# Kernel optimization log

Hardware: AMD Instinct MI355X
Metric: run time of the kernel (lower is better)

## Reference

```python
import jax, jax.numpy as jnp
import numpy as np

G, N, D, K, OUT = 2048, 64, 128, 128, 10  # K*D == input_dim == 16384

def setup_inputs() -> dict:
    key = jax.random.key(0)
    k1, k2, k3, k4, k5 = jax.random.split(key, 5)
    x = jax.random.normal(k1, (G, N, D), dtype=jnp.float32)
    # nn.Linear(node_dim, input_dim/node_dim): weight [K, D], bias [K]
    W_att = jax.random.normal(k2, (K, D), dtype=jnp.float32) * (1.0 / np.sqrt(D))
    b_att = jax.random.normal(k3, (K,), dtype=jnp.float32) * 0.01
    # nn.Linear(input_dim, output_dim): weight [OUT, K*D], bias [OUT]
    W1 = jax.random.normal(k4, (OUT, K * D), dtype=jnp.float32) * (1.0 / np.sqrt(K * D))
    b1 = jax.random.normal(k5, (OUT,), dtype=jnp.float32) * 0.01
    return {"x": x, "W_att": W_att, "b_att": b_att, "W1": W1, "b1": b1}

def reference(x, W_att, b_att, W1, b1):
    # Per-graph gram matrix X^T X : [G, D, D], quantized to 2 decimals
    gram = jnp.einsum('gnd,gne->gde', x, x)
    gram = jnp.round(gram * 100.0) / 100.0
    # attend: Linear(D -> K) applied row-wise to gram -> attn_coef [G, D, K]
    attn = jnp.einsum('gde,ke->gdk', gram, W_att) + b_att
    # attn_weights = attn^T ([G, K, D]); pooled = attn_weights @ gram -> [G, K, D]
    pooled = jnp.einsum('gdk,gde->gke', attn, gram)
    flat = pooled.reshape(x.shape[0], K * D)  # view(input_dim)
    # linear1 (dropout omitted: eval mode)
    return flat @ W1.T + b1
```

## Files before the change

### kernel.cpp

```cpp
#include <hip/hip_runtime.h>

typedef __attribute__((ext_vector_type(8)))  __bf16    bf16x8;
typedef __attribute__((ext_vector_type(4)))  __bf16    bf16x4;
typedef __attribute__((ext_vector_type(16))) float     f32x16;
typedef __attribute__((ext_vector_type(4)))  _Float16  f16x4;
typedef __attribute__((ext_vector_type(2)))  __fp16    h16x2;
typedef __attribute__((ext_vector_type(8)))  __fp16    h16x8;

constexpr int NG  = 2048;
constexpr int NN  = 64;
constexpr int DD  = 128;
constexpr int KK  = 128;
constexpr int OUTD = 10;

__device__ __host__ inline void tileOf(int t, int& ti, int& tj) {
    if (t < 4)      { ti = 0; tj = t;     }
    else if (t < 7) { ti = 1; tj = t - 3; }
    else if (t < 9) { ti = 2; tj = t - 5; }
    else            { ti = 3; tj = 3;     }
}

__device__ inline int xtIdx(int r, int c) { return r * 64  + (c ^ ((r & 7) << 3)); }
__device__ inline int gIdx (int r, int c) { return r * 128 + (c ^ ((r & 15) << 3)); }

#if __has_builtin(__builtin_amdgcn_fdot2)
__device__ __forceinline__ float dot2f(h16x2 a, h16x2 b, float c) {
    return __builtin_amdgcn_fdot2(a, b, c, false);
}
#else
__device__ __forceinline__ float dot2f(h16x2 a, h16x2 b, float c) {
    return c + (float)a[0] * (float)b[0] + (float)a[1] * (float)b[1];
}
#endif

__global__ __launch_bounds__(256)
void fused_sp_kernel(const float* __restrict__ Wa,
                     const float* __restrict__ b_att,
                     const float* __restrict__ W1,
                     _Float16* __restrict__ Sp,
                     float* __restrict__ cgout)
{
    const int blk = blockIdx.x;
    const int o = blk / 10, t = blk - o * 10;
    int ti, tj; tileOf(t, ti, tj);
    const int Fi = ti * 32, Ej = tj * 32;
    const float* __restrict__ W1o = W1 + (size_t)o * (KK * DD);

    __shared__ float WaF[KK][32];
    __shared__ float WaE[KK][32];
    __shared__ float W1F[KK][32];
    __shared__ float W1E[KK][32];
    __shared__ float AFE[32][33];
    __shared__ float AEF[32][33];
    __shared__ float bsh[KK];

    const int tid = threadIdx.x;

    for (int r0 = 0; r0 < KK; r0 += 8) {
        const int r = r0 + (tid >> 5), cc = tid & 31;
        WaF[r][cc] = Wa[r * DD + Fi + cc];
        WaE[r][cc] = Wa[r * DD + Ej + cc];
        W1F[r][cc] = W1o[r * DD + Fi + cc];
        W1E[r][cc] = W1o[r * DD + Ej + cc];
    }
    if (tid < KK) bsh[tid] = b_att[tid];
    __syncthreads();

    {
        const int rloc = tid >> 3;
        const int q    = (tid & 7) * 4;
        float a0 = 0.f, a1 = 0.f, a2 = 0.f, a3 = 0.f;
        float b0 = 0.f, b1 = 0.f, b2 = 0.f, b3 = 0.f;
        for (int k = 0; k < KK; ++k) {
            const float av = WaF[k][rloc];
            const float4 wv = *(const float4*)&W1E[k][q];
            a0 += av * wv.x; a1 += av * wv.y; a2 += av * wv.z; a3 += av * wv.w;
            const float bv = WaE[k][rloc];
            const float4 vv = *(const float4*)&W1F[k][q];
            b0 += bv * vv.x; b1 += bv * vv.y; b2 += bv * vv.z; b3 += bv * vv.w;
        }
        AFE[rloc][q] = a0; AFE[rloc][q + 1] = a1; AFE[rloc][q + 2] = a2; AFE[rloc][q + 3] = a3;
        AEF[rloc][q] = b0; AEF[rloc][q + 1] = b1; AEF[rloc][q + 2] = b2; AEF[rloc][q + 3] = b3;
    }
    __syncthreads();

    {
        const int l  = tid & 63;
        const int rq = tid >> 6;
        const int eg = l & 31;
        const int e  = Ej + eg;
        f16x4 p;
#pragma unroll
        for (int j = 0; j < 4; ++j) {
            const int fl = j + 8 * rq + 4 * (l >> 5);
            const int f  = Fi + fl;
            float v;
            if (f < e)       v = AFE[fl][eg] + AEF[eg][fl];
            else if (f == e) v = AFE[fl][eg];
            else             v = 0.f;
            p[j] = (_Float16)v;
        }
        *(f16x4*)&Sp[(size_t)((o * 10 + t) * 64 + l) * 16 + rq * 4] = p;
    }

    if (ti == 0 && tid < 32) {
        float s = 0.f;
        for (int k = 0; k < KK; ++k) s += bsh[k] * W1E[k][tid];
        cgout[o * DD + Ej + tid] = s;
    }
}

__device__ __forceinline__ void process_graph(
    const float* __restrict__ xg,
    __bf16* __restrict__ XtL, __bf16* __restrict__ GL,
    float (*__restrict__ sp)[DD], float* __restrict__ sOut,
    int tid, int w, int l, int l31, int l5, int extraBase,
    f32x16& hacc0, f32x16& haccX)
{
    {
        const int f = tid & 127, half = tid >> 7;
#pragma unroll
        for (int ch = 0; ch < 2; ++ch) {
            float v[8];
#pragma unroll
            for (int i = 0; i < 8; ++i) v[i] = xg[(half * 16 + ch * 8 + i) * DD + f];
            bf16x8 p;
#pragma unroll
            for (int i = 0; i < 8; ++i) p[i] = (__bf16)v[i];
            *(bf16x8*)&XtL[xtIdx(f, half * 16 + ch * 8)] = p;
        }
    }
    __syncthreads();

    const int ti  = w & 3;
    const int tj0 = (w >> 2) * 2;
    f32x16 acc0, acc1;
#pragma unroll
    for (int i = 0; i < 16; ++i) { acc0[i] = 0.f; acc1[i] = 0.f; }
    {
        const int arow  = ti  * 32 + l31;
        const int brow0 = tj0 * 32 + l31;
#pragma unroll
        for (int ks = 0; ks < 4; ++ks) {
            const int kc = ks * 16 + l5 * 8;
            bf16x8 a  = *(const bf16x8*)&XtL[xtIdx(arow, kc)];
            bf16x8 b0 = *(const bf16x8*)&XtL[xtIdx(brow0, kc)];
            bf16x8 b1 = *(const bf16x8*)&XtL[xtIdx(brow0 + 32, kc)];
            acc0 = __builtin_amdgcn_mfma_f32_32x32x16_bf16(a, b0, acc0, 0, 0, 0);
            acc1 = __builtin_amdgcn_mfma_f32_32x32x16_bf16(a, b1, acc1, 0, 0, 0);
        }
    }
    __syncthreads();

    {
        float sum0 = 0.f, sum1 = 0.f;
#pragma unroll
        for (int tt = 0; tt < 2; ++tt) {
            const int e = (tj0 + tt) * 32 + l31;
#pragma unroll
            for (int g2 = 0; g2 < 4; ++g2) {
                bf16x4 p;
#pragma unroll
                for (int j = 0; j < 4; ++j) {
                    const float av = tt ? acc1[g2 * 4 + j] : acc0[g2 * 4 + j];
                    const float q = rintf(av * 100.f) * 0.01f;
                    p[j] = (__bf16)q;
                    if (tt) sum1 += q; else sum0 += q;
                }
                const int fbase = ti * 32 + g2 * 8 + l5 * 4;
                *(bf16x4*)&GL[gIdx(e, fbase)] = p;
            }
        }
        sp[ti * 2 + l5][tj0 * 32 + l31]       = sum0;
        sp[ti * 2 + l5][(tj0 + 1) * 32 + l31] = sum1;
    }
    __syncthreads();

    if (w == 2 || w == 3) {
        const int e = (w - 2) * 64 + l;
        float s = 0.f;
#pragma unroll
        for (int i = 0; i < 8; ++i) s += sp[i][e];
        sOut[e] = s;
    }

#pragma unroll
    for (int i = 0; i < 16; ++i) hacc0[i] = 0.f;
    {
        int hti, htj; tileOf(w, hti, htj);
        const int ra = hti * 32 + l31, rb = htj * 32 + l31;
#pragma unroll
        for (int ks = 0; ks < 8; ++ks) {
            const int kc = ks * 16 + l5 * 8;
            bf16x8 a = *(const bf16x8*)&GL[gIdx(ra, kc)];
            bf16x8 b = *(const bf16x8*)&GL[gIdx(rb, kc)];
            hacc0 = __builtin_amdgcn_mfma_f32_32x32x16_bf16(a, b, hacc0, 0, 0, 0);
        }
    }
    if (w == extraBase || w == extraBase + 1) {
        int ti1, tj1; tileOf(8 + (w - extraBase), ti1, tj1);
        const int ra = ti1 * 32 + l31, rb = tj1 * 32 + l31;
#pragma unroll
        for (int ks = 0; ks < 8; ++ks) {
            const int kc = ks * 16 + l5 * 8;
            bf16x8 a = *(const bf16x8*)&GL[gIdx(ra, kc)];
            bf16x8 b = *(const bf16x8*)&GL[gIdx(rb, kc)];
            haccX = __builtin_amdgcn_mfma_f32_32x32x16_bf16(a, b, haccX, 0, 0, 0);
        }
    }
    __syncthreads();
}

__global__ __launch_bounds__(512)
void graph_kernel(const float* __restrict__ x,
                  const _Float16* __restrict__ Sp,
                  const float* __restrict__ cg,
                  const float* __restrict__ bias1,
                  float* __restrict__ out)
{
    __shared__ __align__(16) char ldsraw[20 * 512 * 4];
    __shared__ float sp[8][DD];
    __shared__ float sA[DD], sB[DD];

    __bf16* const XtL = (__bf16*)ldsraw;
    __bf16* const GL  = (__bf16*)ldsraw;
    float*  const PP  = (float*)ldsraw;

    const int g0  = blockIdx.x * 2;
    const int g1  = g0 + 1;
    const int tid = threadIdx.x;
    const int w   = tid >> 6;
    const int l   = tid & 63;
    const int l31 = l & 31;
    const int l5  = l >> 5;

    f32x16 hA0, hB0, hX1;
#pragma unroll
    for (int i = 0; i < 16; ++i) hX1[i] = 0.f;

    process_graph(x + (size_t)g0 * NN * DD, XtL, GL, sp, sA,
                  tid, w, l, l31, l5, 6, hA0, hX1);
    process_graph(x + (size_t)g1 * NN * DD, XtL, GL, sp, sB,
                  tid, w, l, l31, l5, 4, hB0, hX1);

    h16x2 hA[8], hB[8], hX[8];
#pragma unroll
    for (int i = 0; i < 8; ++i) {
        hA[i] = __builtin_amdgcn_cvt_pkrtz(hA0[2 * i], hA0[2 * i + 1]);
        hB[i] = __builtin_amdgcn_cvt_pkrtz(hB0[2 * i], hB0[2 * i + 1]);
        hX[i] = __builtin_amdgcn_cvt_pkrtz(hX1[2 * i], hX1[2 * i + 1]);
    }

#pragma unroll
    for (int o = 0; o < OUTD; ++o) {
        const _Float16* __restrict__ spp = Sp + (size_t)((o * 10 + w) * 64 + l) * 16;
        const h16x8 s0 = *(const h16x8*)&spp[0];
        const h16x8 s1 = *(const h16x8*)&spp[8];
        float tA = 0.f, tB = 0.f;
#pragma unroll
        for (int i = 0; i < 4; ++i) {
            const h16x2 p = { s0[2 * i], s0[2 * i + 1] };
            tA = dot2f(p, hA[i], tA);
            tB = dot2f(p, hB[i], tB);
        }
#pragma unroll
        for (int i = 0; i < 4; ++i) {
            const h16x2 p = { s1[2 * i], s1[2 * i + 1] };
            tA = dot2f(p, hA[4 + i], tA);
            tB = dot2f(p, hB[4 + i], tB);
        }
        if (w >= 4) {
            const _Float16* __restrict__ sp2 =
                Sp + (size_t)((o * 10 + 8 + (w & 1)) * 64 + l) * 16;
            const h16x8 e0 = *(const h16x8*)&sp2[0];
            const h16x8 e1 = *(const h16x8*)&sp2[8];
            float tx = 0.f;
#pragma unroll
            for (int i = 0; i < 4; ++i) {
                const h16x2 p = { e0[2 * i], e0[2 * i + 1] };
                tx = dot2f(p, hX[i], tx);
            }
#pragma unroll
            for (int i = 0; i < 4; ++i) {
                const h16x2 p = { e1[2 * i], e1[2 * i + 1] };
                tx = dot2f(p, hX[4 + i], tx);
            }
            if (w >= 6) tA += tx; else tB += tx;
        }
        if (w == 0) {
            tA += cg[o * DD + l] * sA[l] + cg[o * DD + 64 + l] * sA[64 + l];
            tB += cg[o * DD + l] * sB[l] + cg[o * DD + 64 + l] * sB[64 + l];
        }
        PP[o * 512 + tid]        = tA;
        PP[(10 + o) * 512 + tid] = tB;
    }
    __syncthreads();

    for (int p = w; p < 2 * OUTD; p += 8) {
        const float4 q0 = *(const float4*)&PP[p * 512 + l * 8];
        const float4 q1 = *(const float4*)&PP[p * 512 + l * 8 + 4];
        float v = (q0.x + q0.y) + (q0.z + q0.w) + (q1.x + q1.y) + (q1.z + q1.w);
        v += __shfl_down(v, 32, 64);
        v += __shfl_down(v, 16, 64);
        v += __shfl_down(v, 8, 64);
        v += __shfl_down(v, 4, 64);
        v += __shfl_down(v, 2, 64);
        v += __shfl_down(v, 1, 64);
        if (l == 0) {
            const int gg = (p < OUTD) ? g0 : g1;
            const int oo = (p < OUTD) ? p : p - OUTD;
            out[(size_t)gg * OUTD + oo] = v + bias1[oo];
        }
    }
}

extern "C" void kernel_launch(void* const* d_in, const int* in_sizes, int n_in,
                              void* d_out, int out_size, void* d_ws, size_t ws_size,
                              hipStream_t stream)
{
    const float* x     = (const float*)d_in[0];
    const float* Wa    = (const float*)d_in[1];
    const float* b_att = (const float*)d_in[2];
    const float* W1    = (const float*)d_in[3];
    const float* bias1 = (const float*)d_in[4];
    float* out = (float*)d_out;

    float*    cg = (float*)d_ws;
    _Float16* Sp = (_Float16*)(cg + OUTD * DD);

    fused_sp_kernel<<<100, 256, 0, stream>>>(Wa, b_att, W1, Sp, cg);
    graph_kernel<<<NG / 2, 512, 0, stream>>>(x, Sp, cg, bias1, out);
}
```

Measured before the change: 43.23 us.

## Overlap second graph's global load with first graph's gram computation

Inlines the two per-graph passes and gives XtL and GL separate LDS regions. Graph B's input is prefetched into registers while graph A's X^T X MFMA runs, then written to LDS alongside A's quantized gram. This removes one barrier and hides part of B's global-load latency. In exchange, LDS use grows to 48KB plus 16 more live float registers per thread, which may lower occupancy.

After: 42.75 us. Within noise of the previous version (-1.1%).

```diff
diff --git a/kernel.cpp b/kernel.cpp
--- a/kernel.cpp
+++ b/kernel.cpp
@@ -110,107 +110,6 @@
     }
 }
 
-__device__ __forceinline__ void process_graph(
-    const float* __restrict__ xg,
-    __bf16* __restrict__ XtL, __bf16* __restrict__ GL,
-    float (*__restrict__ sp)[DD], float* __restrict__ sOut,
-    int tid, int w, int l, int l31, int l5, int extraBase,
-    f32x16& hacc0, f32x16& haccX)
-{
-    {
-        const int f = tid & 127, half = tid >> 7;
-#pragma unroll
-        for (int ch = 0; ch < 2; ++ch) {
-            float v[8];
-#pragma unroll
-            for (int i = 0; i < 8; ++i) v[i] = xg[(half * 16 + ch * 8 + i) * DD + f];
-            bf16x8 p;
-#pragma unroll
-            for (int i = 0; i < 8; ++i) p[i] = (__bf16)v[i];
-            *(bf16x8*)&XtL[xtIdx(f, half * 16 + ch * 8)] = p;
-        }
-    }
-    __syncthreads();
-
-    const int ti  = w & 3;
-    const int tj0 = (w >> 2) * 2;
-    f32x16 acc0, acc1;
-#pragma unroll
-    for (int i = 0; i < 16; ++i) { acc0[i] = 0.f; acc1[i] = 0.f; }
-    {
-        const int arow  = ti  * 32 + l31;
-        const int brow0 = tj0 * 32 + l31;
-#pragma unroll
-        for (int ks = 0; ks < 4; ++ks) {
-            const int kc = ks * 16 + l5 * 8;
-            bf16x8 a  = *(const bf16x8*)&XtL[xtIdx(arow, kc)];
-            bf16x8 b0 = *(const bf16x8*)&XtL[xtIdx(brow0, kc)];
-            bf16x8 b1 = *(const bf16x8*)&XtL[xtIdx(brow0 + 32, kc)];
-            acc0 = __builtin_amdgcn_mfma_f32_32x32x16_bf16(a, b0, acc0, 0, 0, 0);
-            acc1 = __builtin_amdgcn_mfma_f32_32x32x16_bf16(a, b1, acc1, 0, 0, 0);
-        }
-    }
-    __syncthreads();
-
-    {
-        float sum0 = 0.f, sum1 = 0.f;
-#pragma unroll
-        for (int tt = 0; tt < 2; ++tt) {
-            const int e = (tj0 + tt) * 32 + l31;
-#pragma unroll
-            for (int g2 = 0; g2 < 4; ++g2) {
-                bf16x4 p;
-#pragma unroll
-                for (int j = 0; j < 4; ++j) {
-                    const float av = tt ? acc1[g2 * 4 + j] : acc0[g2 * 4 + j];
-                    const float q = rintf(av * 100.f) * 0.01f;
-                    p[j] = (__bf16)q;
-                    if (tt) sum1 += q; else sum0 += q;
-                }
-                const int fbase = ti * 32 + g2 * 8 + l5 * 4;
-                *(bf16x4*)&GL[gIdx(e, fbase)] = p;
-            }
-        }
-        sp[ti * 2 + l5][tj0 * 32 + l31]       = sum0;
-        sp[ti * 2 + l5][(tj0 + 1) * 32 + l31] = sum1;
-    }
-    __syncthreads();
-
-    if (w == 2 || w == 3) {
-        const int e = (w - 2) * 64 + l;
-        float s = 0.f;
-#pragma unroll
-        for (int i = 0; i < 8; ++i) s += sp[i][e];
-        sOut[e] = s;
-    }
-
-#pragma unroll
-    for (int i = 0; i < 16; ++i) hacc0[i] = 0.f;
-    {
-        int hti, htj; tileOf(w, hti, htj);
-        const int ra = hti * 32 + l31, rb = htj * 32 + l31;
-#pragma unroll
-        for (int ks = 0; ks < 8; ++ks) {
-            const int kc = ks * 16 + l5 * 8;
-            bf16x8 a = *(const bf16x8*)&GL[gIdx(ra, kc)];
-            bf16x8 b = *(const bf16x8*)&GL[gIdx(rb, kc)];
-            hacc0 = __builtin_amdgcn_mfma_f32_32x32x16_bf16(a, b, hacc0, 0, 0, 0);
-        }
-    }
-    if (w == extraBase || w == extraBase + 1) {
-        int ti1, tj1; tileOf(8 + (w - extraBase), ti1, tj1);
-        const int ra = ti1 * 32 + l31, rb = tj1 * 32 + l31;
-#pragma unroll
-        for (int ks = 0; ks < 8; ++ks) {
-            const int kc = ks * 16 + l5 * 8;
-            bf16x8 a = *(const bf16x8*)&GL[gIdx(ra, kc)];
-            bf16x8 b = *(const bf16x8*)&GL[gIdx(rb, kc)];
-            haccX = __builtin_amdgcn_mfma_f32_32x32x16_bf16(a, b, haccX, 0, 0, 0);
-        }
-    }
-    __syncthreads();
-}
-
 __global__ __launch_bounds__(512)
 void graph_kernel(const float* __restrict__ x,
                   const _Float16* __restrict__ Sp,
@@ -218,12 +117,12 @@
                   const float* __restrict__ bias1,
                   float* __restrict__ out)
 {
-    __shared__ __align__(16) char ldsraw[20 * 512 * 4];
+    __shared__ __align__(16) char ldsraw[48 * 1024];
     __shared__ float sp[8][DD];
     __shared__ float sA[DD], sB[DD];
 
     __bf16* const XtL = (__bf16*)ldsraw;
-    __bf16* const GL  = (__bf16*)ldsraw;
+    __bf16* const GL  = (__bf16*)(ldsraw + 16 * 1024);
     float*  const PP  = (float*)ldsraw;
 
     const int g0  = blockIdx.x * 2;
@@ -233,15 +132,186 @@
     const int l   = tid & 63;
     const int l31 = l & 31;
     const int l5  = l >> 5;
+    const int f   = tid & 127, half = tid >> 7;
+    const float* __restrict__ xgA = x + (size_t)g0 * NN * DD;
+    const float* __restrict__ xgB = x + (size_t)g1 * NN * DD;
+
+    const int ti  = w & 3;
+    const int tj0 = (w >> 2) * 2;
+
+    {
+#pragma unroll
+        for (int ch = 0; ch < 2; ++ch) {
+            float v[8];
+#pragma unroll
+            for (int i = 0; i < 8; ++i) v[i] = xgA[(half * 16 + ch * 8 + i) * DD + f];
+            bf16x8 p;
+#pragma unroll
+            for (int i = 0; i < 8; ++i) p[i] = (__bf16)v[i];
+            *(bf16x8*)&XtL[xtIdx(f, half * 16 + ch * 8)] = p;
+        }
+    }
+    __syncthreads();
+
+    float vB[16];
+#pragma unroll
+    for (int i = 0; i < 16; ++i) vB[i] = xgB[(half * 16 + i) * DD + f];
 
     f32x16 hA0, hB0, hX1;
 #pragma unroll
     for (int i = 0; i < 16; ++i) hX1[i] = 0.f;
 
-    process_graph(x + (size_t)g0 * NN * DD, XtL, GL, sp, sA,
-                  tid, w, l, l31, l5, 6, hA0, hX1);
-    process_graph(x + (size_t)g1 * NN * DD, XtL, GL, sp, sB,
-                  tid, w, l, l31, l5, 4, hB0, hX1);
+    f32x16 acc0, acc1;
+#pragma unroll
+    for (int i = 0; i < 16; ++i) { acc0[i] = 0.f; acc1[i] = 0.f; }
+    {
+        const int arow  = ti  * 32 + l31;
+        const int brow0 = tj0 * 32 + l31;
+#pragma unroll
+        for (int ks = 0; ks < 4; ++ks) {
+            const int kc = ks * 16 + l5 * 8;
+            bf16x8 a  = *(const bf16x8*)&XtL[xtIdx(arow, kc)];
+            bf16x8 b0 = *(const bf16x8*)&XtL[xtIdx(brow0, kc)];
+            bf16x8 b1 = *(const bf16x8*)&XtL[xtIdx(brow0 + 32, kc)];
+            acc0 = __builtin_amdgcn_mfma_f32_32x32x16_bf16(a, b0, acc0, 0, 0, 0);
+            acc1 = __builtin_amdgcn_mfma_f32_32x32x16_bf16(a, b1, acc1, 0, 0, 0);
+        }
+    }
+    __syncthreads();
+
+    {
+        float sum0 = 0.f, sum1 = 0.f;
+#pragma unroll
+        for (int tt = 0; tt < 2; ++tt) {
+            const int e = (tj0 + tt) * 32 + l31;
+#pragma unroll
+            for (int g2 = 0; g2 < 4; ++g2) {
+                bf16x4 p;
+#pragma unroll
+                for (int j = 0; j < 4; ++j) {
+                    const float av = tt ? acc1[g2 * 4 + j] : acc0[g2 * 4 + j];
+                    const float q = rintf(av * 100.f) * 0.01f;
+                    p[j] = (__bf16)q;
+                    if (tt) sum1 += q; else sum0 += q;
+                }
+                *(bf16x4*)&GL[gIdx(e, ti * 32 + g2 * 8 + l5 * 4)] = p;
+            }
+        }
+        sp[ti * 2 + l5][tj0 * 32 + l31]       = sum0;
+        sp[ti * 2 + l5][(tj0 + 1) * 32 + l31] = sum1;
+    }
+    {
+        bf16x8 p0, p1;
+#pragma unroll
+        for (int i = 0; i < 8; ++i) { p0[i] = (__bf16)vB[i]; p1[i] = (__bf16)vB[8 + i]; }
+        *(bf16x8*)&XtL[xtIdx(f, half * 16)]     = p0;
+        *(bf16x8*)&XtL[xtIdx(f, half * 16 + 8)] = p1;
+    }
+    __syncthreads();
+
+    if (w == 2 || w == 3) {
+        const int e = (w - 2) * 64 + l;
+        float s = 0.f;
+#pragma unroll
+        for (int i = 0; i < 8; ++i) s += sp[i][e];
+        sA[e] = s;
+    }
+#pragma unroll
+    for (int i = 0; i < 16; ++i) hA0[i] = 0.f;
+    {
+        int hti, htj; tileOf(w, hti, htj);
+        const int ra = hti * 32 + l31, rb = htj * 32 + l31;
+#pragma unroll
+        for (int ks = 0; ks < 8; ++ks) {
+            const int kc = ks * 16 + l5 * 8;
+            bf16x8 a = *(const bf16x8*)&GL[gIdx(ra, kc)];
+            bf16x8 b = *(const bf16x8*)&GL[gIdx(rb, kc)];
+            hA0 = __builtin_amdgcn_mfma_f32_32x32x16_bf16(a, b, hA0, 0, 0, 0);
+        }
+    }
+    if (w >= 6) {
+        int ti1, tj1; tileOf(8 + (w - 6), ti1, tj1);
+        const int ra = ti1 * 32 + l31, rb = tj1 * 32 + l31;
+#pragma unroll
+        for (int ks = 0; ks < 8; ++ks) {
+            const int kc = ks * 16 + l5 * 8;
+            bf16x8 a = *(const bf16x8*)&GL[gIdx(ra, kc)];
+            bf16x8 b = *(const bf16x8*)&GL[gIdx(rb, kc)];
+            hX1 = __builtin_amdgcn_mfma_f32_32x32x16_bf16(a, b, hX1, 0, 0, 0);
+        }
+    }
+    __syncthreads();
+
+#pragma unroll
+    for (int i = 0; i < 16; ++i) { acc0[i] = 0.f; acc1[i] = 0.f; }
+    {
+        const int arow  = ti  * 32 + l31;
+        const int brow0 = tj0 * 32 + l31;
+#pragma unroll
+        for (int ks = 0; ks < 4; ++ks) {
+            const int kc = ks * 16 + l5 * 8;
+            bf16x8 a  = *(const bf16x8*)&XtL[xtIdx(arow, kc)];
+            bf16x8 b0 = *(const bf16x8*)&XtL[xtIdx(brow0, kc)];
+            bf16x8 b1 = *(const bf16x8*)&XtL[xtIdx(brow0 + 32, kc)];
+            acc0 = __builtin_amdgcn_mfma_f32_32x32x16_bf16(a, b0, acc0, 0, 0, 0);
+            acc1 = __builtin_amdgcn_mfma_f32_32x32x16_bf16(a, b1, acc1, 0, 0, 0);
+        }
+    }
+    {
+        float sum0 = 0.f, sum1 = 0.f;
+#pragma unroll
+        for (int tt = 0; tt < 2; ++tt) {
+            const int e = (tj0 + tt) * 32 + l31;
+#pragma unroll
+            for (int g2 = 0; g2 < 4; ++g2) {
+                bf16x4 p;
+#pragma unroll
+                for (int j = 0; j < 4; ++j) {
+                    const float av = tt ? acc1[g2 * 4 + j] : acc0[g2 * 4 + j];
+                    const float q = rintf(av * 100.f) * 0.01f;
+                    p[j] = (__bf16)q;
+                    if (tt) sum1 += q; else sum0 += q;
+                }
+                *(bf16x4*)&GL[gIdx(e, ti * 32 + g2 * 8 + l5 * 4)] = p;
+            }
+        }
+        sp[ti * 2 + l5][tj0 * 32 + l31]       = sum0;
+        sp[ti * 2 + l5][(tj0 + 1) * 32 + l31] = sum1;
+    }
+    __syncthreads();
+
+    if (w == 2 || w == 3) {
+        const int e = (w - 2) * 64 + l;
+        float s = 0.f;
+#pragma unroll
+        for (int i = 0; i < 8; ++i) s += sp[i][e];
+        sB[e] = s;
+    }
+#pragma unroll
+    for (int i = 0; i < 16; ++i) hB0[i] = 0.f;
+    {
+        int hti, htj; tileOf(w, hti, htj);
+        const int ra = hti * 32 + l31, rb = htj * 32 + l31;
+#pragma unroll
+        for (int ks = 0; ks < 8; ++ks) {
+            const int kc = ks * 16 + l5 * 8;
+            bf16x8 a = *(const bf16x8*)&GL[gIdx(ra, kc)];
+            bf16x8 b = *(const bf16x8*)&GL[gIdx(rb, kc)];
+            hB0 = __builtin_amdgcn_mfma_f32_32x32x16_bf16(a, b, hB0, 0, 0, 0);
+        }
+    }
+    if (w == 4 || w == 5) {
+        int ti1, tj1; tileOf(8 + (w - 4), ti1, tj1);
+        const int ra = ti1 * 32 + l31, rb = tj1 * 32 + l31;
+#pragma unroll
+        for (int ks = 0; ks < 8; ++ks) {
+            const int kc = ks * 16 + l5 * 8;
+            bf16x8 a = *(const bf16x8*)&GL[gIdx(ra, kc)];
+            bf16x8 b = *(const bf16x8*)&GL[gIdx(rb, kc)];
+            hX1 = __builtin_amdgcn_mfma_f32_32x32x16_bf16(a, b, hX1, 0, 0, 0);
+        }
+    }
+    __syncthreads();
 
     h16x2 hA[8], hB[8], hX[8];
 #pragma unroll
```
